# Kernel tuning notes

Hardware: AMD Instinct MI355X
Metric: run time of the kernel (lower is better)

Reference implementation:

```python
import jax, jax.numpy as jnp
import numpy as np

FM = 64            # feature_maps
PASS_STEPS = 3
OUT_BITS = 16


def _linear(x, w, b):
    return x @ w + b


def _mlp(x, w1, b1, w2, b2):
    return _linear(jax.nn.relu(_linear(x, w1, b1)), w2, b2)


def setup_inputs() -> dict:
    key = jax.random.key(0)
    ks = jax.random.split(key, 20)
    VAR, CON, NNZ = 100000, 50000, 2000000

    def w(k, i, o):
        return jax.random.normal(k, (i, o), dtype=jnp.float32) * 0.05

    inp = {
        "row_idx": jax.random.randint(ks[0], (NNZ,), 0, VAR),
        "col_idx": jax.random.randint(ks[1], (NNZ,), 0, CON),
        "adj_vals": jax.random.normal(ks[2], (NNZ,), dtype=jnp.float32),
        "conditions_values": jax.random.normal(ks[3], (CON,), dtype=jnp.float32),
        "var_count": VAR,
        "const_count": CON,
        # prepare_cond: 1 -> 2*FM -> FM
        "pc_w1": w(ks[4], 1, 2 * FM), "pc_b1": jnp.zeros((2 * FM,), jnp.float32),
        "pc_w2": w(ks[5], 2 * FM, FM), "pc_b2": jnp.zeros((FM,), jnp.float32),
        # constraint_update: 2*FM -> 2*FM -> FM
        "cu_w1": w(ks[6], 2 * FM, 2 * FM), "cu_b1": jnp.zeros((2 * FM,), jnp.float32),
        "cu_w2": w(ks[7], 2 * FM, FM), "cu_b2": jnp.zeros((FM,), jnp.float32),
        # variable_update: 2*FM -> 2*FM -> FM
        "vu_w1": w(ks[8], 2 * FM, 2 * FM), "vu_b1": jnp.zeros((2 * FM,), jnp.float32),
        "vu_w2": w(ks[9], 2 * FM, FM), "vu_b2": jnp.zeros((FM,), jnp.float32),
        # output: FM -> 2*FM -> OUT_BITS
        "out_w1": w(ks[10], FM, 2 * FM), "out_b1": jnp.zeros((2 * FM,), jnp.float32),
        "out_w2": w(ks[11], 2 * FM, OUT_BITS), "out_b2": jnp.zeros((OUT_BITS,), jnp.float32),
    }
    return inp


def reference(row_idx, col_idx, adj_vals, conditions_values, var_count, const_count,
              pc_w1, pc_b1, pc_w2, pc_b2,
              cu_w1, cu_b1, cu_w2, cu_b2,
              vu_w1, vu_b1, vu_w2, vu_b2,
              out_w1, out_b1, out_w2, out_b2):
    vals = jnp.abs(adj_vals)                                   # [nnz]
    variables = jnp.ones((var_count, FM), dtype=jnp.float32)   # [V, FM]
    constraints = _mlp(conditions_values[:, None], pc_w1, pc_b1, pc_w2, pc_b2)  # [C, FM]

    for _ in range(PASS_STEPS):
        # var -> const: A^T @ variables  (gather rows, scatter-add to cols)
        v2c = jax.ops.segment_sum(vals[:, None] * variables[row_idx],
                                  col_idx, num_segments=const_count)   # [C, FM]
        constraints = _mlp(jnp.concatenate([constraints, v2c], axis=-1),
                           cu_w1, cu_b1, cu_w2, cu_b2)
        # const -> var: A @ constraints
        c2v = jax.ops.segment_sum(vals[:, None] * constraints[col_idx],
                                  row_idx, num_segments=var_count)     # [V, FM]
        variables = _mlp(jnp.concatenate([variables, c2v], axis=-1),
                         vu_w1, vu_b1, vu_w2, vu_b2)

    return jax.nn.sigmoid(_mlp(variables, out_w1, out_b1, out_w2, out_b2))  # [V, OUT_BITS]
```

## Files before the change

### kernel.cpp

```cpp
#include <hip/hip_runtime.h>
#include <hip/hip_fp16.h>

typedef unsigned int uint;

#define GB_D 64
#define MS_CH 16384
#define BS_CAP 6912

using h8  = __attribute__((ext_vector_type(8))) _Float16;
using h4  = __attribute__((ext_vector_type(4))) _Float16;
using f4v = __attribute__((ext_vector_type(4))) float;

__device__ __forceinline__ float4 ld4(const float* p) { return *reinterpret_cast<const float4*>(p); }
__device__ __forceinline__ void st4(float* p, float4 v) { *reinterpret_cast<float4*>(p) = v; }
__device__ __forceinline__ void fma4(float4& a, float s, const float4 w) {
    a.x = fmaf(s, w.x, a.x); a.y = fmaf(s, w.y, a.y);
    a.z = fmaf(s, w.z, a.z); a.w = fmaf(s, w.w, a.w);
}
__device__ __forceinline__ uint pk2(float a, float b) {
    __half2 h = __floats2half2_rn(a, b);
    return *reinterpret_cast<uint*>(&h);
}

__global__ __launch_bounds__(256) void k_bhist(const int* __restrict__ row, const int* __restrict__ col,
                                               int nnz, int* __restrict__ bcnt, int nbc, int nbt) {
    extern __shared__ int ls[];
    for (int b = threadIdx.x; b < nbt; b += blockDim.x) ls[b] = 0;
    __syncthreads();
    int i0 = blockIdx.x * blockDim.x + threadIdx.x;
    int stride = gridDim.x * blockDim.x;
    for (int i = i0; i < nnz; i += stride) {
        atomicAdd(&ls[col[i] >> 6], 1);
        atomicAdd(&ls[nbc + (row[i] >> 6)], 1);
    }
    __syncthreads();
    for (int b = threadIdx.x; b < nbt; b += blockDim.x) {
        int c = ls[b];
        if (c) atomicAdd(&bcnt[b], c);
    }
}

__global__ __launch_bounds__(1024) void k_bscan(const int* __restrict__ cnt, int n,
                                                int* __restrict__ ptr, int* __restrict__ nxt) {
    __shared__ int wsum[17];
    __shared__ int carry, tot;
    if (threadIdx.x == 0) carry = 0;
    __syncthreads();
    int lane = threadIdx.x & 63;
    int wid  = threadIdx.x >> 6;
    for (int base = 0; base < n; base += 1024) {
        int idx = base + (int)threadIdx.x;
        int v = (idx < n) ? cnt[idx] : 0;
        int inc = v;
        #pragma unroll
        for (int off = 1; off < 64; off <<= 1) {
            int t = __shfl_up(inc, (unsigned)off, 64);
            if (lane >= off) inc += t;
        }
        if (lane == 63) wsum[wid] = inc;
        __syncthreads();
        if (threadIdx.x == 0) {
            int s = 0;
            for (int w = 0; w < 16; w++) { int t = wsum[w]; wsum[w] = s; s += t; }
            tot = s;
        }
        __syncthreads();
        int excl = carry + wsum[wid] + (inc - v);
        if (idx < n) { ptr[idx] = excl; nxt[idx] = excl; }
        __syncthreads();
        if (threadIdx.x == 0) carry += tot;
        __syncthreads();
    }
    if (threadIdx.x == 0) ptr[n] = carry;
}

__global__ __launch_bounds__(256) void k_mpsplit(const int* __restrict__ row, const int* __restrict__ col,
                                                 const float* __restrict__ adj, int nnz,
                                                 int* __restrict__ bnxt, int2* __restrict__ pack,
                                                 int nbc, int nbt) {
    extern __shared__ int ls[];
    const int t = threadIdx.x;
    for (int b = t; b < nbt; b += 256) ls[b] = 0;
    __syncthreads();
    const int start = blockIdx.x * MS_CH;
    const int end = min(start + MS_CH, nnz);
    for (int i = start + t; i < end; i += 256) {
        atomicAdd(&ls[col[i] >> 6], 1);
        atomicAdd(&ls[nbc + (row[i] >> 6)], 1);
    }
    __syncthreads();
    for (int b = t; b < nbt; b += 256) {
        int c = ls[b];
        ls[b] = c ? atomicAdd(&bnxt[b], c) : 0;
    }
    __syncthreads();
    for (int i = start + t; i < end; i += 256) {
        int r = row[i], c = col[i];
        int vb = __float_as_int(fabsf(adj[i]));
        int p1 = atomicAdd(&ls[c >> 6], 1);
        pack[p1] = make_int2(((c & 63) << 20) | r, vb);
        int p2 = atomicAdd(&ls[nbc + (r >> 6)], 1);
        pack[p2] = make_int2(((r & 63) << 20) | c, vb);
    }
}

__global__ __launch_bounds__(256) void k_bsort(const int* __restrict__ bptr, int2* __restrict__ pack,
                                               int* __restrict__ dptr_c, int C,
                                               int* __restrict__ dptr_v, int V, int nbc) {
    __shared__ int2 ebuf[BS_CAP];
    __shared__ int h[GB_D];
    __shared__ int cur[GB_D];
    const int b = blockIdx.x, t = threadIdx.x;
    const int s = bptr[b], e = bptr[b + 1];
    const int n = min(e - s, BS_CAP);
    if (t < GB_D) h[t] = 0;
    __syncthreads();
    for (int i = t; i < n; i += 256) {
        int2 ed = pack[s + i];
        ebuf[i] = ed;
        atomicAdd(&h[((uint)ed.x) >> 20], 1);
    }
    __syncthreads();
    if (t < GB_D) {
        int v = h[t];
        int inc = v;
        #pragma unroll
        for (int off = 1; off < 64; off <<= 1) {
            int u = __shfl_up(inc, (unsigned)off, 64);
            if (t >= off) inc += u;
        }
        int excl = inc - v;
        cur[t] = excl;
        const bool isC = (b < nbc);
        const int base = (isC ? b : b - nbc) << 6;
        const int nd   = isC ? C : V;
        int* dp        = isC ? dptr_c : dptr_v;
        const int d = base + t;
        if (d < nd) dp[d] = s + excl;
        if (d == nd - 1) dp[nd] = s + n;
    }
    __syncthreads();
    for (int i = t; i < n; i += 256) {
        int2 ed = ebuf[i];
        int p = atomicAdd(&cur[((uint)ed.x) >> 20], 1);
        pack[s + p] = make_int2(ed.x & 0xFFFFF, ed.y);
    }
}

__global__ __launch_bounds__(256) void k_gather(const int* __restrict__ dptr,
                                                const int2* __restrict__ es,
                                                const __half* __restrict__ sfeat,
                                                float* __restrict__ dmsg, int n) {
    int wid = (int)((blockIdx.x * blockDim.x + threadIdx.x) >> 6);
    int lane = threadIdx.x & 63;
    int nw = (int)((gridDim.x * blockDim.x) >> 6);
    for (int d = wid; d < n; d += nw) {
        int s = dptr[d], e = dptr[d + 1];
        float a0 = 0.f, a1 = 0.f, a2 = 0.f, a3 = 0.f;
        int i = s;
        for (; i + 3 < e; i += 4) {
            int2 e0 = es[i], e1 = es[i + 1], e2 = es[i + 2], e3 = es[i + 3];
            a0 = fmaf(__int_as_float(e0.y), __half2float(sfeat[(size_t)e0.x * 64 + lane]), a0);
            a1 = fmaf(__int_as_float(e1.y), __half2float(sfeat[(size_t)e1.x * 64 + lane]), a1);
            a2 = fmaf(__int_as_float(e2.y), __half2float(sfeat[(size_t)e2.x * 64 + lane]), a2);
            a3 = fmaf(__int_as_float(e3.y), __half2float(sfeat[(size_t)e3.x * 64 + lane]), a3);
        }
        for (; i < e; i++) {
            int2 e0 = es[i];
            a0 = fmaf(__int_as_float(e0.y), __half2float(sfeat[(size_t)e0.x * 64 + lane]), a0);
        }
        dmsg[(size_t)d * 64 + lane] = (a0 + a1) + (a2 + a3);
    }
}

__global__ __launch_bounds__(256) void k_ones2(float4* p, int n4, uint4* ph, int n4h) {
    int i0 = blockIdx.x * blockDim.x + threadIdx.x;
    int stride = gridDim.x * blockDim.x;
    float4 one = make_float4(1.f, 1.f, 1.f, 1.f);
    uint4 oneh = make_uint4(0x3C003C00u, 0x3C003C00u, 0x3C003C00u, 0x3C003C00u);
    for (int i = i0; i < n4; i += stride) p[i] = one;
    for (int i = i0; i < n4h; i += stride) ph[i] = oneh;
}

__global__ __launch_bounds__(256) void k_pc2(const float* __restrict__ cond, float* __restrict__ constraints,
                                             __half* __restrict__ conh, int C,
                                             const float* __restrict__ w1, const float* __restrict__ b1,
                                             const float* __restrict__ w2, const float* __restrict__ b2) {
    __shared__ float hs[64][132];
    __shared__ float cs[64];
    const int t = threadIdx.x;
    const int base = blockIdx.x * 64;
    const int rem = C - base;

    if (t < 64) cs[t] = (t < rem) ? cond[base + t] : 0.f;
    __syncthreads();

    #pragma unroll
    for (int j = 0; j < 32; j++) {
        int idx = j * 256 + t;
        int k = idx & 127, row = idx >> 7;
        hs[row][k] = fmaxf(fmaf(cs[row], w1[k], b1[k]), 0.f);
    }
    __syncthreads();

    const int tx2 = t & 15, ty2 = t >> 4;
    float4 bb = ld4(b2 + tx2 * 4);
    float4 acc[4] = { bb, bb, bb, bb };
    const float* w2p = w2 + tx2 * 4;
    #pragma unroll 4
    for (int k = 0; k < 128; k++) {
        float4 w = ld4(w2p + k * 64);
        fma4(acc[0], hs[ty2 * 4 + 0][k], w);
        fma4(acc[1], hs[ty2 * 4 + 1][k], w);
        fma4(acc[2], hs[ty2 * 4 + 2][k], w);
        fma4(acc[3], hs[ty2 * 4 + 3][k], w);
    }
    #pragma unroll
    for (int r = 0; r < 4; r++) {
        int row = ty2 * 4 + r;
        if (row < rem) {
            st4(&constraints[(size_t)(base + row) * 64 + tx2 * 4], acc[r]);
            uint2 o;
            o.x = pk2(acc[r].x, acc[r].y);
            o.y = pk2(acc[r].z, acc[r].w);
            *(uint2*)(conh + (size_t)(base + row) * 64 + tx2 * 4) = o;
        }
    }
}

__global__ __launch_bounds__(256) void k_mlp3(float* __restrict__ feat, const float* __restrict__ msg,
                                              __half* __restrict__ mirror, int n,
                                              const float* __restrict__ w1, const float* __restrict__ b1,
                                              const float* __restrict__ w2, const float* __restrict__ b2) {
    __shared__ _Float16 xh[64][136];
    __shared__ _Float16 xl[64][136];
    const int t = threadIdx.x;
    const int base = blockIdx.x * 64;
    const int rem = n - base;
    const int wv = t >> 6;
    const int la = t & 15;
    const int lb = (t & 63) >> 4;

    {
        const float4* f4p = (const float4*)(feat + (size_t)base * 64);
        const float4* m4p = (const float4*)(msg + (size_t)base * 64);
        #pragma unroll
        for (int j = 0; j < 8; j++) {
            int idx = j * 256 + t;
            int row = idx >> 5;
            int q   = idx & 31;
            float4 v = make_float4(0.f, 0.f, 0.f, 0.f);
            if (row < rem) v = (q < 16) ? f4p[row * 16 + q] : m4p[row * 16 + (q - 16)];
            int k = (q < 16) ? q * 4 : 64 + (q - 16) * 4;
            h4 hi, lo;
            hi[0] = (_Float16)v.x; lo[0] = (_Float16)(v.x - (float)hi[0]);
            hi[1] = (_Float16)v.y; lo[1] = (_Float16)(v.y - (float)hi[1]);
            hi[2] = (_Float16)v.z; lo[2] = (_Float16)(v.z - (float)hi[2]);
            hi[3] = (_Float16)v.w; lo[3] = (_Float16)(v.w - (float)hi[3]);
            *(h4*)&xh[row][k] = hi;
            *(h4*)&xl[row][k] = lo;
        }
    }

    h8 B1[2][4];
    h8 B2[4];
    #pragma unroll
    for (int nn = 0; nn < 2; nn++) {
        int col = wv * 32 + nn * 16 + la;
        #pragma unroll
        for (int kc = 0; kc < 4; kc++) {
            int kb = kc * 32 + lb * 8;
            h8 bb;
            #pragma unroll
            for (int j = 0; j < 8; j++) bb[j] = (_Float16)w1[(kb + j) * 128 + col];
            B1[nn][kc] = bb;
        }
    }
    {
        int col = wv * 16 + la;
        #pragma unroll
        for (int kc = 0; kc < 4; kc++) {
            int kb = kc * 32 + lb * 8;
            h8 bb;
            #pragma unroll
            for (int j = 0; j < 8; j++) bb[j] = (_Float16)w2[(kb + j) * 64 + col];
            B2[kc] = bb;
        }
    }
    const float b1v0 = b1[wv * 32 + la];
    const float b1v1 = b1[wv * 32 + 16 + la];
    const float b2v  = b2[wv * 16 + la];

    __syncthreads();

    f4v acc[4][2];
    #pragma unroll
    for (int r = 0; r < 4; r++) {
        f4v z = {0.f, 0.f, 0.f, 0.f};
        acc[r][0] = z; acc[r][1] = z;
    }
    #pragma unroll
    for (int r = 0; r < 4; r++) {
        h8 Ah[4], Al[4];
        #pragma unroll
        for (int kc = 0; kc < 4; kc++) {
            Ah[kc] = *(const h8*)&xh[r * 16 + la][kc * 32 + lb * 8];
            Al[kc] = *(const h8*)&xl[r * 16 + la][kc * 32 + lb * 8];
        }
        #pragma unroll
        for (int nn = 0; nn < 2; nn++) {
            #pragma unroll
            for (int kc = 0; kc < 4; kc++) {
                acc[r][nn] = __builtin_amdgcn_mfma_f32_16x16x32_f16(Ah[kc], B1[nn][kc], acc[r][nn], 0, 0, 0);
                acc[r][nn] = __builtin_amdgcn_mfma_f32_16x16x32_f16(Al[kc], B1[nn][kc], acc[r][nn], 0, 0, 0);
            }
        }
    }
    __syncthreads();

    #pragma unroll
    for (int r = 0; r < 4; r++) {
        #pragma unroll
        for (int nn = 0; nn < 2; nn++) {
            const float bv = nn ? b1v1 : b1v0;
            const int col = wv * 32 + nn * 16 + la;
            #pragma unroll
            for (int i = 0; i < 4; i++) {
                float h = fmaxf(acc[r][nn][i] + bv, 0.f);
                int row = r * 16 + lb * 4 + i;
                _Float16 hh = (_Float16)h;
                xh[row][col] = hh;
                xl[row][col] = (_Float16)(h - (float)hh);
            }
        }
    }
    __syncthreads();

    f4v acc2[4];
    #pragma unroll
    for (int r = 0; r < 4; r++) { f4v z = {0.f, 0.f, 0.f, 0.f}; acc2[r] = z; }
    #pragma unroll
    for (int r = 0; r < 4; r++) {
        h8 Ah[4], Al[4];
        #pragma unroll
        for (int kc = 0; kc < 4; kc++) {
            Ah[kc] = *(const h8*)&xh[r * 16 + la][kc * 32 + lb * 8];
            Al[kc] = *(const h8*)&xl[r * 16 + la][kc * 32 + lb * 8];
        }
        #pragma unroll
        for (int kc = 0; kc < 4; kc++) {
            acc2[r] = __builtin_amdgcn_mfma_f32_16x16x32_f16(Ah[kc], B2[kc], acc2[r], 0, 0, 0);
            acc2[r] = __builtin_amdgcn_mfma_f32_16x16x32_f16(Al[kc], B2[kc], acc2[r], 0, 0, 0);
        }
    }

    {
        const int col = wv * 16 + la;
        #pragma unroll
        for (int r = 0; r < 4; r++) {
            #pragma unroll
            for (int i = 0; i < 4; i++) {
                int row = r * 16 + lb * 4 + i;
                if (row < rem) {
                    float y = acc2[r][i] + b2v;
                    size_t idx = (size_t)(base + row) * 64 + col;
                    feat[idx] = y;
                    mirror[idx] = __float2half_rn(y);
                }
            }
        }
    }
}

__global__ __launch_bounds__(256) void k_out2(const float* __restrict__ vars, float* __restrict__ out, int V,
                                              const float* __restrict__ w1, const float* __restrict__ b1,
                                              const float* __restrict__ w2, const float* __restrict__ b2) {
    __shared__ float xs[64][68];
    __shared__ float hs[64][132];
    const int t = threadIdx.x;
    const int base = blockIdx.x * 64;
    const int rem = V - base;

    {
        const float4* v4 = (const float4*)(vars + (size_t)base * 64);
        #pragma unroll
        for (int j = 0; j < 4; j++) {
            int idx = j * 256 + t;
            int row = idx >> 4;
            int kq  = idx & 15;
            float4 v = (row < rem) ? v4[row * 16 + kq] : make_float4(0, 0, 0, 0);
            xs[kq * 4 + 0][row] = v.x; xs[kq * 4 + 1][row] = v.y;
            xs[kq * 4 + 2][row] = v.z; xs[kq * 4 + 3][row] = v.w;
        }
    }
    __syncthreads();

    const int tx = t & 31, ty = t >> 5;
    {
        float4 bb = ld4(b1 + tx * 4);
        float4 acc[8];
        #pragma unroll
        for (int r = 0; r < 8; r++) acc[r] = bb;
        const float* w1p = w1 + tx * 4;
        #pragma unroll 4
        for (int k = 0; k < 64; k++) {
            float4 w  = ld4(w1p + k * 128);
            float4 xa = ld4(&xs[k][ty * 8]);
            float4 xb = ld4(&xs[k][ty * 8 + 4]);
            fma4(acc[0], xa.x, w); fma4(acc[1], xa.y, w);
            fma4(acc[2], xa.z, w); fma4(acc[3], xa.w, w);
            fma4(acc[4], xb.x, w); fma4(acc[5], xb.y, w);
            fma4(acc[6], xb.z, w); fma4(acc[7], xb.w, w);
        }
        #pragma unroll
        for (int r = 0; r < 8; r++) {
            float4 h;
            h.x = fmaxf(acc[r].x, 0.f); h.y = fmaxf(acc[r].y, 0.f);
            h.z = fmaxf(acc[r].z, 0.f); h.w = fmaxf(acc[r].w, 0.f);
            st4(&hs[ty * 8 + r][tx * 4], h);
        }
    }
    __syncthreads();

    const int tx3 = t & 3, ty3 = t >> 2;
    {
        float4 o = ld4(b2 + tx3 * 4);
        const float* w2p = w2 + tx3 * 4;
        #pragma unroll 4
        for (int k = 0; k < 128; k++) {
            float4 w = ld4(w2p + k * 16);
            fma4(o, hs[ty3][k], w);
        }
        o.x = 1.f / (1.f + __expf(-o.x));
        o.y = 1.f / (1.f + __expf(-o.y));
        o.z = 1.f / (1.f + __expf(-o.z));
        o.w = 1.f / (1.f + __expf(-o.w));
        if (ty3 < rem) st4(&out[(size_t)(base + ty3) * 16 + tx3 * 4], o);
    }
}


extern "C" void kernel_launch(void* const* d_in, const int* in_sizes, int n_in,
                              void* d_out, int out_size, void* d_ws, size_t ws_size,
                              hipStream_t stream) {
    const int*   row_idx = (const int*)d_in[0];
    const int*   col_idx = (const int*)d_in[1];
    const float* adj     = (const float*)d_in[2];
    const float* cond    = (const float*)d_in[3];
    const float* pc_w1  = (const float*)d_in[6];
    const float* pc_b1  = (const float*)d_in[7];
    const float* pc_w2  = (const float*)d_in[8];
    const float* pc_b2  = (const float*)d_in[9];
    const float* cu_w1  = (const float*)d_in[10];
    const float* cu_b1  = (const float*)d_in[11];
    const float* cu_w2  = (const float*)d_in[12];
    const float* cu_b2  = (const float*)d_in[13];
    const float* vu_w1  = (const float*)d_in[14];
    const float* vu_b1  = (const float*)d_in[15];
    const float* vu_w2  = (const float*)d_in[16];
    const float* vu_b2  = (const float*)d_in[17];
    const float* out_w1 = (const float*)d_in[18];
    const float* out_b1 = (const float*)d_in[19];
    const float* out_w2 = (const float*)d_in[20];
    const float* out_b2 = (const float*)d_in[21];

    const int NNZ = in_sizes[0];
    const int C   = in_sizes[3];
    const int V   = out_size / 16;

    const int NBc = (C + GB_D - 1) / GB_D;
    const int NBv = (V + GB_D - 1) / GB_D;
    const int NBT = NBc + NBv;

    float* out = (float*)d_out;

    char* wsb = (char*)d_ws;
    size_t off = 0;
    auto carve = [&](size_t bytes) -> void* {
        void* p = wsb + off;
        off = (off + bytes + 255) & ~(size_t)255;
        return p;
    };
    float*  variables   = (float*)carve((size_t)V * 64 * 4);
    float*  constraints = (float*)carve((size_t)C * 64 * 4);
    float*  v2c         = (float*)carve((size_t)C * 64 * 4);
    float*  c2v         = (float*)carve((size_t)V * 64 * 4);
    __half* var_h       = (__half*)carve((size_t)V * 64 * 2);
    __half* con_h       = (__half*)carve((size_t)C * 64 * 2);
    int2*   pack        = (int2*)carve((size_t)2 * NNZ * 8);
    int*    bcnt        = (int*)carve((size_t)NBT * 4);
    int*    bptr        = (int*)carve((size_t)(NBT + 1) * 4);
    int*    bnxt        = (int*)carve((size_t)NBT * 4);
    int*    dptr_c      = (int*)carve((size_t)(C + 1) * 4);
    int*    dptr_v      = (int*)carve((size_t)(V + 1) * 4);
    (void)ws_size; (void)n_in;

    const size_t shmem = (size_t)NBT * 4;

    hipMemsetAsync(bcnt, 0, (size_t)NBT * 4, stream);
    k_bhist<<<256, 256, shmem, stream>>>(row_idx, col_idx, NNZ, bcnt, NBc, NBT);
    k_bscan<<<1, 1024, 0, stream>>>(bcnt, NBT, bptr, bnxt);
    k_mpsplit<<<(NNZ + MS_CH - 1) / MS_CH, 256, shmem, stream>>>(row_idx, col_idx, adj, NNZ,
                                                                 bnxt, pack, NBc, NBT);
    k_bsort<<<NBT, 256, 0, stream>>>(bptr, pack, dptr_c, C, dptr_v, V, NBc);

    k_ones2<<<2048, 256, 0, stream>>>((float4*)variables, V * 16, (uint4*)var_h, V * 8);
    k_pc2<<<(C + 63) / 64, 256, 0, stream>>>(cond, constraints, con_h, C, pc_w1, pc_b1, pc_w2, pc_b2);

    for (int p = 0; p < 3; p++) {
        k_gather<<<2048, 256, 0, stream>>>(dptr_c, pack, var_h, v2c, C);
        k_mlp3<<<(C + 63) / 64, 256, 0, stream>>>(constraints, v2c, con_h, C, cu_w1, cu_b1, cu_w2, cu_b2);
        k_gather<<<2048, 256, 0, stream>>>(dptr_v, pack, con_h, c2v, V);
        k_mlp3<<<(V + 63) / 64, 256, 0, stream>>>(variables, c2v, var_h, V, vu_w1, vu_b1, vu_w2, vu_b2);
    }

    k_out2<<<(V + 63) / 64, 256, 0, stream>>>(variables, out, V, out_w1, out_b1, out_w2, out_b2);
}
```

Measured before the change: 909.1 us.

## Use split-fp16 MFMA for output MLP and unroll gather by eight

The output MLP kernel is rewritten to run on MFMA matrix instructions. Activations are split into fp16 high and low parts so the products keep near-fp32 accuracy, while the weights are simply rounded to fp16. The gather kernel's edge loop is unrolled to eight independent accumulators to expose more memory-level parallelism. The partition chunk size is also halved to launch more blocks in the sort stage. The weight rounding adds a small precision loss, and the extra accumulators raise register pressure.

Measured after the change: 823.2 us. 1.1x faster.

```diff
diff --git a/kernel.cpp b/kernel.cpp
--- a/kernel.cpp
+++ b/kernel.cpp
@@ -4,7 +4,7 @@
 typedef unsigned int uint;
 
 #define GB_D 64
-#define MS_CH 16384
+#define MS_CH 8192
 #define BS_CAP 6912
 
 using h8  = __attribute__((ext_vector_type(8))) _Float16;
@@ -157,19 +157,30 @@
     for (int d = wid; d < n; d += nw) {
         int s = dptr[d], e = dptr[d + 1];
         float a0 = 0.f, a1 = 0.f, a2 = 0.f, a3 = 0.f;
+        float a4 = 0.f, a5 = 0.f, a6 = 0.f, a7 = 0.f;
         int i = s;
-        for (; i + 3 < e; i += 4) {
-            int2 e0 = es[i], e1 = es[i + 1], e2 = es[i + 2], e3 = es[i + 3];
+        for (; i + 7 < e; i += 8) {
+            int2 e0 = es[i],     e1 = es[i + 1], e2 = es[i + 2], e3 = es[i + 3];
+            int2 e4 = es[i + 4], e5 = es[i + 5], e6 = es[i + 6], e7 = es[i + 7];
             a0 = fmaf(__int_as_float(e0.y), __half2float(sfeat[(size_t)e0.x * 64 + lane]), a0);
             a1 = fmaf(__int_as_float(e1.y), __half2float(sfeat[(size_t)e1.x * 64 + lane]), a1);
             a2 = fmaf(__int_as_float(e2.y), __half2float(sfeat[(size_t)e2.x * 64 + lane]), a2);
             a3 = fmaf(__int_as_float(e3.y), __half2float(sfeat[(size_t)e3.x * 64 + lane]), a3);
-        }
-        for (; i < e; i++) {
+            a4 = fmaf(__int_as_float(e4.y), __half2float(sfeat[(size_t)e4.x * 64 + lane]), a4);
+            a5 = fmaf(__int_as_float(e5.y), __half2float(sfeat[(size_t)e5.x * 64 + lane]), a5);
+            a6 = fmaf(__int_as_float(e6.y), __half2float(sfeat[(size_t)e6.x * 64 + lane]), a6);
+            a7 = fmaf(__int_as_float(e7.y), __half2float(sfeat[(size_t)e7.x * 64 + lane]), a7);
+        }
+        for (; i + 1 < e; i += 2) {
+            int2 e0 = es[i], e1 = es[i + 1];
+            a0 = fmaf(__int_as_float(e0.y), __half2float(sfeat[(size_t)e0.x * 64 + lane]), a0);
+            a1 = fmaf(__int_as_float(e1.y), __half2float(sfeat[(size_t)e1.x * 64 + lane]), a1);
+        }
+        if (i < e) {
             int2 e0 = es[i];
             a0 = fmaf(__int_as_float(e0.y), __half2float(sfeat[(size_t)e0.x * 64 + lane]), a0);
         }
-        dmsg[(size_t)d * 64 + lane] = (a0 + a1) + (a2 + a3);
+        dmsg[(size_t)d * 64 + lane] = ((a0 + a1) + (a2 + a3)) + ((a4 + a5) + (a6 + a7));
     }
 }
 
@@ -372,70 +383,134 @@
     }
 }
 
-__global__ __launch_bounds__(256) void k_out2(const float* __restrict__ vars, float* __restrict__ out, int V,
+__global__ __launch_bounds__(256) void k_out3(const float* __restrict__ vars, float* __restrict__ out, int V,
                                               const float* __restrict__ w1, const float* __restrict__ b1,
                                               const float* __restrict__ w2, const float* __restrict__ b2) {
-    __shared__ float xs[64][68];
-    __shared__ float hs[64][132];
+    __shared__ _Float16 xh[64][136];
+    __shared__ _Float16 xl[64][136];
     const int t = threadIdx.x;
     const int base = blockIdx.x * 64;
     const int rem = V - base;
+    const int wv = t >> 6;
+    const int la = t & 15;
+    const int lb = (t & 63) >> 4;
 
     {
-        const float4* v4 = (const float4*)(vars + (size_t)base * 64);
+        const float4* v4p = (const float4*)(vars + (size_t)base * 64);
         #pragma unroll
         for (int j = 0; j < 4; j++) {
             int idx = j * 256 + t;
             int row = idx >> 4;
-            int kq  = idx & 15;
-            float4 v = (row < rem) ? v4[row * 16 + kq] : make_float4(0, 0, 0, 0);
-            xs[kq * 4 + 0][row] = v.x; xs[kq * 4 + 1][row] = v.y;
-            xs[kq * 4 + 2][row] = v.z; xs[kq * 4 + 3][row] = v.w;
-        }
-    }
-    __syncthreads();
-
-    const int tx = t & 31, ty = t >> 5;
+            int q   = idx & 15;
+            float4 v = make_float4(0.f, 0.f, 0.f, 0.f);
+            if (row < rem) v = v4p[row * 16 + q];
+            int k = q * 4;
+            h4 hi, lo;
+            hi[0] = (_Float16)v.x; lo[0] = (_Float16)(v.x - (float)hi[0]);
+            hi[1] = (_Float16)v.y; lo[1] = (_Float16)(v.y - (float)hi[1]);
+            hi[2] = (_Float16)v.z; lo[2] = (_Float16)(v.z - (float)hi[2]);
+            hi[3] = (_Float16)v.w; lo[3] = (_Float16)(v.w - (float)hi[3]);
+            *(h4*)&xh[row][k] = hi;
+            *(h4*)&xl[row][k] = lo;
+        }
+    }
+
+    h8 B1[2][2];
+    h8 B2[4];
+    #pragma unroll
+    for (int nn = 0; nn < 2; nn++) {
+        int col = wv * 32 + nn * 16 + la;
+        #pragma unroll
+        for (int kc = 0; kc < 2; kc++) {
+            int kb = kc * 32 + lb * 8;
+            h8 bb;
+            #pragma unroll
+            for (int j = 0; j < 8; j++) bb[j] = (_Float16)w1[(kb + j) * 128 + col];
+            B1[nn][kc] = bb;
+        }
+    }
     {
-        float4 bb = ld4(b1 + tx * 4);
-        float4 acc[8];
-        #pragma unroll
-        for (int r = 0; r < 8; r++) acc[r] = bb;
-        const float* w1p = w1 + tx * 4;
-        #pragma unroll 4
-        for (int k = 0; k < 64; k++) {
-            float4 w  = ld4(w1p + k * 128);
-            float4 xa = ld4(&xs[k][ty * 8]);
-            float4 xb = ld4(&xs[k][ty * 8 + 4]);
-            fma4(acc[0], xa.x, w); fma4(acc[1], xa.y, w);
-            fma4(acc[2], xa.z, w); fma4(acc[3], xa.w, w);
-            fma4(acc[4], xb.x, w); fma4(acc[5], xb.y, w);
-            fma4(acc[6], xb.z, w); fma4(acc[7], xb.w, w);
-        }
-        #pragma unroll
-        for (int r = 0; r < 8; r++) {
-            float4 h;
-            h.x = fmaxf(acc[r].x, 0.f); h.y = fmaxf(acc[r].y, 0.f);
-            h.z = fmaxf(acc[r].z, 0.f); h.w = fmaxf(acc[r].w, 0.f);
-            st4(&hs[ty * 8 + r][tx * 4], h);
-        }
-    }
-    __syncthreads();
-
-    const int tx3 = t & 3, ty3 = t >> 2;
+        int col = la;
+        #pragma unroll
+        for (int kc = 0; kc < 4; kc++) {
+            int kb = kc * 32 + lb * 8;
+            h8 bb;
+            #pragma unroll
+            for (int j = 0; j < 8; j++) bb[j] = (_Float16)w2[(kb + j) * 16 + col];
+            B2[kc] = bb;
+        }
+    }
+    const float b1v0 = b1[wv * 32 + la];
+    const float b1v1 = b1[wv * 32 + 16 + la];
+    const float b2v  = b2[la];
+
+    __syncthreads();
+
+    f4v acc[4][2];
+    #pragma unroll
+    for (int r = 0; r < 4; r++) {
+        f4v z = {0.f, 0.f, 0.f, 0.f};
+        acc[r][0] = z; acc[r][1] = z;
+    }
+    #pragma unroll
+    for (int r = 0; r < 4; r++) {
+        h8 Ah[2], Al[2];
+        #pragma unroll
+        for (int kc = 0; kc < 2; kc++) {
+            Ah[kc] = *(const h8*)&xh[r * 16 + la][kc * 32 + lb * 8];
+            Al[kc] = *(const h8*)&xl[r * 16 + la][kc * 32 + lb * 8];
+        }
+        #pragma unroll
+        for (int nn = 0; nn < 2; nn++) {
+            #pragma unroll
+            for (int kc = 0; kc < 2; kc++) {
+                acc[r][nn] = __builtin_amdgcn_mfma_f32_16x16x32_f16(Ah[kc], B1[nn][kc], acc[r][nn], 0, 0, 0);
+                acc[r][nn] = __builtin_amdgcn_mfma_f32_16x16x32_f16(Al[kc], B1[nn][kc], acc[r][nn], 0, 0, 0);
+            }
+        }
+    }
+    __syncthreads();
+
+    #pragma unroll
+    for (int r = 0; r < 4; r++) {
+        #pragma unroll
+        for (int nn = 0; nn < 2; nn++) {
+            const float bv = nn ? b1v1 : b1v0;
+            const int col = wv * 32 + nn * 16 + la;
+            #pragma unroll
+            for (int i = 0; i < 4; i++) {
+                float h = fmaxf(acc[r][nn][i] + bv, 0.f);
+                int row = r * 16 + lb * 4 + i;
+                _Float16 hh = (_Float16)h;
+                xh[row][col] = hh;
+                xl[row][col] = (_Float16)(h - (float)hh);
+            }
+        }
+    }
+    __syncthreads();
+
+    f4v acc2 = {0.f, 0.f, 0.f, 0.f};
     {
-        float4 o = ld4(b2 + tx3 * 4);
-        const float* w2p = w2 + tx3 * 4;
-        #pragma unroll 4
-        for (int k = 0; k < 128; k++) {
-            float4 w = ld4(w2p + k * 16);
-            fma4(o, hs[ty3][k], w);
-        }
-        o.x = 1.f / (1.f + __expf(-o.x));
-        o.y = 1.f / (1.f + __expf(-o.y));
-        o.z = 1.f / (1.f + __expf(-o.z));
-        o.w = 1.f / (1.f + __expf(-o.w));
-        if (ty3 < rem) st4(&out[(size_t)(base + ty3) * 16 + tx3 * 4], o);
+        h8 Ah[4], Al[4];
+        #pragma unroll
+        for (int kc = 0; kc < 4; kc++) {
+            Ah[kc] = *(const h8*)&xh[wv * 16 + la][kc * 32 + lb * 8];
+            Al[kc] = *(const h8*)&xl[wv * 16 + la][kc * 32 + lb * 8];
+        }
+        #pragma unroll
+        for (int kc = 0; kc < 4; kc++) {
+            acc2 = __builtin_amdgcn_mfma_f32_16x16x32_f16(Ah[kc], B2[kc], acc2, 0, 0, 0);
+            acc2 = __builtin_amdgcn_mfma_f32_16x16x32_f16(Al[kc], B2[kc], acc2, 0, 0, 0);
+        }
+    }
+
+    #pragma unroll
+    for (int i = 0; i < 4; i++) {
+        int row = wv * 16 + lb * 4 + i;
+        if (row < rem) {
+            float y = acc2[i] + b2v;
+            out[(size_t)(base + row) * 16 + la] = 1.f / (1.f + __expf(-y));
+        }
     }
 }
 
@@ -514,5 +589,5 @@
         k_mlp3<<<(V + 63) / 64, 256, 0, stream>>>(variables, c2v, var_h, V, vu_w1, vu_b1, vu_w2, vu_b2);
     }
 
-    k_out2<<<(V + 63) / 64, 256, 0, stream>>>(variables, out, V, out_w1, out_b1, out_w2, out_b2);
-}
+    k_out3<<<(V + 63) / 64, 256, 0, stream>>>(variables, out, V, out_w1, out_b1, out_w2, out_b2);
+}
```
